# Kernel optimization log

Measured on AMD Instinct MI355X. Metric: run time of the kernel, lower is better.

## Reference

```python
import jax, jax.numpy as jnp
import numpy as np

NEVENTS = 100000
EMB_DIM = 64
NCONDS = 50
BATCH = 16384


def setup_inputs() -> dict:
    key = jax.random.key(0)
    k_idx, k_tab = jax.random.split(key)
    inp = jax.random.randint(k_idx, (BATCH, 1 + NCONDS), 0, NEVENTS + 2, dtype=jnp.int64 if jax.config.jax_enable_x64 else jnp.int32)
    event_table = jax.random.normal(k_tab, (NEVENTS + 2, EMB_DIM), dtype=jnp.float32)
    return {"input": inp, "event_table": event_table}


def reference(input, event_table):
    # Note: original module defines cond_embedding but uses event_embedding for both lookups.
    event = input[:, 0:1]          # [B, 1]
    conditions = input[:, 1:]      # [B, C]
    event_emb = event_table[event]        # [B, 1, D]
    cond_emb = event_table[conditions]    # [B, C, D]
    # L2 normalize along last dim (torch .norm(dim=2, keepdim=True))
    event_nrm = event_emb / jnp.linalg.norm(event_emb, axis=2, keepdims=True)
    cond_nrm = cond_emb / jnp.linalg.norm(cond_emb, axis=2, keepdims=True)
    # scores: [B, 1, C] = event_nrm @ cond_nrm^T
    scores = jnp.einsum('bod,bcd->boc', event_nrm, cond_nrm)
    # filtered_cond: [B, C, D] = cond_nrm * scores.transpose(1,2) (broadcast over D)
    filtered_cond = cond_nrm * jnp.swapaxes(scores, 1, 2)
    B = input.shape[0]
    return jnp.concatenate((event_emb.reshape(B, -1), filtered_cond.reshape(B, -1)), axis=1)
```

## Files before the change

### kernel.cpp

```cpp
#include <hip/hip_runtime.h>

#define NCONDS 50
#define EMB 64
#define ROW_STRIDE (1 + NCONDS)
#define OUT_STRIDE ((1 + NCONDS) * EMB)

__global__ __launch_bounds__(256) void cond_filter_kernel(
    const int*   __restrict__ inp,
    const float* __restrict__ table,
    float*       __restrict__ out,
    int batch)
{
    const int wave = threadIdx.x >> 6;
    const int lane = threadIdx.x & 63;
    const int b = blockIdx.x * 4 + wave;
    if (b >= batch) return;

    const int grp = lane >> 4;
    const int gl  = lane & 15;

    const int* row = inp + (size_t)b * ROW_STRIDE;
    const int e_idx = row[0];

    const float4 ev = *(const float4*)(table + (size_t)e_idx * EMB + gl * 4);

    float es = ev.x*ev.x + ev.y*ev.y + ev.z*ev.z + ev.w*ev.w;
    #pragma unroll
    for (int m = 1; m < 16; m <<= 1) es += __shfl_xor(es, m, 64);
    const float e_rn = rsqrtf(es);
    const float4 en = make_float4(ev.x*e_rn, ev.y*e_rn, ev.z*e_rn, ev.w*e_rn);

    float* orow = out + (size_t)b * OUT_STRIDE;
    if (grp == 0) {
        *(float4*)(orow + gl * 4) = ev;
    }

    #pragma unroll 1
    for (int base = 0; base < NCONDS; base += 4) {
        const int c = base + grp;
        const bool active = (c < NCONDS);
        const int ci = active ? row[1 + c] : e_idx;

        const float4 cv = *(const float4*)(table + (size_t)ci * EMB + gl * 4);

        float cs = cv.x*cv.x + cv.y*cv.y + cv.z*cv.z + cv.w*cv.w;
        float dp = cv.x*en.x + cv.y*en.y + cv.z*en.z + cv.w*en.w;
        #pragma unroll
        for (int m = 1; m < 16; m <<= 1) {
            cs += __shfl_xor(cs, m, 64);
            dp += __shfl_xor(dp, m, 64);
        }

        const float scale = dp / cs;

        if (active) {
            float4 o = make_float4(cv.x*scale, cv.y*scale, cv.z*scale, cv.w*scale);
            *(float4*)(orow + EMB + (size_t)c * EMB + gl * 4) = o;
        }
    }
}

extern "C" void kernel_launch(void* const* d_in, const int* in_sizes, int n_in,
                              void* d_out, int out_size, void* d_ws, size_t ws_size,
                              hipStream_t stream) {
    const int*   inp   = (const int*)d_in[0];
    const float* table = (const float*)d_in[1];
    float*       out   = (float*)d_out;

    const int batch = in_sizes[0] / ROW_STRIDE;
    const int blocks = (batch + 3) / 4;

    hipLaunchKernelGGL(cond_filter_kernel, dim3(blocks), dim3(256), 0, stream,
                       inp, table, out, batch);
}
```

Before: 256.4 us.

## Prefetch all condition indices and table rows up front, use nontemporal stores

```diff
diff --git a/kernel.cpp b/kernel.cpp
--- a/kernel.cpp
+++ b/kernel.cpp
@@ -4,6 +4,9 @@
 #define EMB 64
 #define ROW_STRIDE (1 + NCONDS)
 #define OUT_STRIDE ((1 + NCONDS) * EMB)
+#define NITER 13
+
+typedef float f4 __attribute__((ext_vector_type(4)));
 
 __global__ __launch_bounds__(256) void cond_filter_kernel(
     const int*   __restrict__ inp,
@@ -20,42 +23,49 @@
     const int gl  = lane & 15;
 
     const int* row = inp + (size_t)b * ROW_STRIDE;
-    const int e_idx = row[0];
+    const int my_idx = (lane < ROW_STRIDE) ? row[lane] : 0;
+    const int e_idx = __shfl(my_idx, 0, 64);
 
-    const float4 ev = *(const float4*)(table + (size_t)e_idx * EMB + gl * 4);
+    int cidx[NITER];
+    #pragma unroll
+    for (int i = 0; i < NITER; ++i) {
+        const int c = i * 4 + grp;
+        const int src = (c < NCONDS) ? (1 + c) : 0;
+        cidx[i] = __shfl(my_idx, src, 64);
+    }
+
+    const f4 ev = *(const f4*)(table + (size_t)e_idx * EMB + gl * 4);
+    f4 cv[NITER];
+    #pragma unroll
+    for (int i = 0; i < NITER; ++i)
+        cv[i] = *(const f4*)(table + (size_t)cidx[i] * EMB + gl * 4);
 
     float es = ev.x*ev.x + ev.y*ev.y + ev.z*ev.z + ev.w*ev.w;
     #pragma unroll
     for (int m = 1; m < 16; m <<= 1) es += __shfl_xor(es, m, 64);
     const float e_rn = rsqrtf(es);
-    const float4 en = make_float4(ev.x*e_rn, ev.y*e_rn, ev.z*e_rn, ev.w*e_rn);
+    const f4 en = ev * e_rn;
 
     float* orow = out + (size_t)b * OUT_STRIDE;
     if (grp == 0) {
-        *(float4*)(orow + gl * 4) = ev;
+        __builtin_nontemporal_store(ev, (f4*)(orow + gl * 4));
     }
 
-    #pragma unroll 1
-    for (int base = 0; base < NCONDS; base += 4) {
-        const int c = base + grp;
-        const bool active = (c < NCONDS);
-        const int ci = active ? row[1 + c] : e_idx;
-
-        const float4 cv = *(const float4*)(table + (size_t)ci * EMB + gl * 4);
-
-        float cs = cv.x*cv.x + cv.y*cv.y + cv.z*cv.z + cv.w*cv.w;
-        float dp = cv.x*en.x + cv.y*en.y + cv.z*en.z + cv.w*en.w;
+    #pragma unroll
+    for (int i = 0; i < NITER; ++i) {
+        const int c = i * 4 + grp;
+        const f4 v = cv[i];
+        float cs = v.x*v.x + v.y*v.y + v.z*v.z + v.w*v.w;
+        float dp = v.x*en.x + v.y*en.y + v.z*en.z + v.w*en.w;
         #pragma unroll
         for (int m = 1; m < 16; m <<= 1) {
             cs += __shfl_xor(cs, m, 64);
             dp += __shfl_xor(dp, m, 64);
         }
-
-        const float scale = dp / cs;
-
-        if (active) {
-            float4 o = make_float4(cv.x*scale, cv.y*scale, cv.z*scale, cv.w*scale);
-            *(float4*)(orow + EMB + (size_t)c * EMB + gl * 4) = o;
+        const float scale = dp * __builtin_amdgcn_rcpf(cs);
+        if (c < NCONDS) {
+            const f4 o = v * scale;
+            __builtin_nontemporal_store(o, (f4*)(orow + EMB + (size_t)c * EMB + gl * 4));
         }
     }
 }
```

Result: faster. 250.1 us (-2.5%).
